# Kernel tuning notes

Measured on AMD Instinct MI355X. Metric: run time of the kernel, lower is better.

Reference implementation:

```python
import jax, jax.numpy as jnp
import numpy as np

N = 50000        # nodes
E = 1600000      # edges
NDIM_IN = 64
HID = 128        # hardcoded hidden width of first SAGELayer in E-GraphSAGE
NDIM_OUT = 128
EDIM = 32
EMBEDIM = 128
NCLASS = 2       # bin=True


def setup_inputs() -> dict:
    key = jax.random.key(0)
    ks = jax.random.split(key, 12)
    g = lambda k, shape: jax.random.normal(k, shape, jnp.float32) / np.sqrt(np.float32(shape[0]))
    return {
        "nfeats": jax.random.normal(ks[0], (N, NDIM_IN), jnp.float32),
        "efeats": jax.random.normal(ks[1], (E, EDIM), jnp.float32),
        "src": jax.random.randint(ks[2], (E,), 0, N),
        "dst": jax.random.randint(ks[3], (E,), 0, N),
        # SAGE layer 1: W_msg [ndim_in+edim -> 128], W_apply [ndim_in+128 -> 128]
        "Wm1": g(ks[4], (NDIM_IN + EDIM, HID)), "bm1": jnp.zeros((HID,), jnp.float32),
        "Wa1": g(ks[5], (NDIM_IN + HID, HID)), "ba1": jnp.zeros((HID,), jnp.float32),
        # SAGE layer 2: W_msg [128+edim -> ndim_out], W_apply [128+ndim_out -> ndim_out]
        "Wm2": g(ks[6], (HID + EDIM, NDIM_OUT)), "bm2": jnp.zeros((NDIM_OUT,), jnp.float32),
        "Wa2": g(ks[7], (HID + NDIM_OUT, NDIM_OUT)), "ba2": jnp.zeros((NDIM_OUT,), jnp.float32),
        # MLPPredictorEmbed: [2*ndim_out -> embedim] -> relu -> [embedim -> 2]
        "W1": g(ks[8], (2 * NDIM_OUT, EMBEDIM)), "b1": jnp.zeros((EMBEDIM,), jnp.float32),
        "W2": g(ks[9], (EMBEDIM, NCLASS)), "b2": jnp.zeros((NCLASS,), jnp.float32),
    }


def _sage_layer(h, efeats, src, dst, Wm, bm, Wa, ba):
    # per-edge message: relu(W_msg([h_src || e]))  -> [E, dout]
    m = jax.nn.relu(jnp.concatenate([h[src], efeats], axis=-1) @ Wm + bm)
    # mean aggregation by destination node (0 for isolated nodes, like DGL fn.mean)
    s = jax.ops.segment_sum(m, dst, num_segments=N)
    cnt = jax.ops.segment_sum(jnp.ones((m.shape[0], 1), m.dtype), dst, num_segments=N)
    h_neigh = s / jnp.maximum(cnt, 1.0)
    # node update: relu(W_apply([h || h_neigh]))
    return jax.nn.relu(jnp.concatenate([h, h_neigh], axis=-1) @ Wa + ba)


def reference(nfeats, efeats, src, dst,
              Wm1, bm1, Wa1, ba1, Wm2, bm2, Wa2, ba2,
              W1, b1, W2, b2):
    h = _sage_layer(nfeats, efeats, src, dst, Wm1, bm1, Wa1, ba1)   # [N, 128]
    h = _sage_layer(h, efeats, src, dst, Wm2, bm2, Wa2, ba2)        # [N, ndim_out]
    # edge predictor: MLP on [h_u || h_v] per edge
    z = jnp.concatenate([h[src], h[dst]], axis=-1)                   # [E, 2*ndim_out]
    score = jax.nn.relu(z @ W1 + b1) @ W2 + b2                       # [E, 2]
    return score
```

## Files before the change

kernel.cpp:

```cpp
#include <hip/hip_runtime.h>

#define N_NODES 50000
#define N_EDGES 1600000

typedef _Float16 h8 __attribute__((ext_vector_type(8)));
typedef float f4 __attribute__((ext_vector_type(4)));

__device__ inline h8 ld_h8(const _Float16* p) { return *(const h8*)p; }

__device__ inline h8 cvt2h8(f4 a, f4 b) {
    h8 r;
    r[0] = (_Float16)a[0]; r[1] = (_Float16)a[1]; r[2] = (_Float16)a[2]; r[3] = (_Float16)a[3];
    r[4] = (_Float16)b[0]; r[5] = (_Float16)b[1]; r[6] = (_Float16)b[2]; r[7] = (_Float16)b[3];
    return r;
}


__global__ void prep_weights(const float* __restrict__ Wm1, const float* __restrict__ Wa1,
                             const float* __restrict__ Wm2, const float* __restrict__ Wa2,
                             const float* __restrict__ W1,
                             _Float16* __restrict__ Wm1t, _Float16* __restrict__ Wa1t,
                             _Float16* __restrict__ Wm2t, _Float16* __restrict__ Wa2t,
                             _Float16* __restrict__ W1t)
{
    int i = blockIdx.x * 256 + threadIdx.x;
    if (i < 12288) {
        int o = i / 96, k = i % 96;
        int ks = k >> 5, q = (k >> 3) & 3, j = k & 7;
        int c = q ^ ((o >> 1) & 3);
        Wm1t[(ks * 128 + o) * 32 + c * 8 + j] = (_Float16)Wm1[k * 128 + o];
    } else if (i < 36864) {
        int jj = i - 12288; int o = jj / 192, k = jj % 192;
        Wa1t[o * 200 + k] = (_Float16)Wa1[k * 128 + o];
    } else if (i < 57344) {
        int jj = i - 36864; int o = jj / 160, k = jj % 160;
        int ks = k >> 5, q = (k >> 3) & 3, j = k & 7;
        int c = q ^ ((o >> 1) & 3);
        Wm2t[(ks * 128 + o) * 32 + c * 8 + j] = (_Float16)Wm2[k * 128 + o];
    } else if (i < 90112) {
        int jj = i - 57344; int o = jj >> 8, k = jj & 255;
        Wa2t[(o << 8) + k] = (_Float16)Wa2[k * 128 + o];
    } else if (i < 122880) {
        int jj = i - 90112; int o = jj >> 8, k = jj & 255;
        W1t[(o << 8) + k] = (_Float16)W1[k * 128 + o];
    }
}

__global__ void cvt_nfeats(const float* __restrict__ nf, _Float16* __restrict__ nf16)
{
    int i = blockIdx.x * 256 + threadIdx.x;
    nf16[i] = (_Float16)nf[i];
}


__global__ void hist_kernel(const int* __restrict__ dst, int* __restrict__ cnt)
{
    int e = blockIdx.x * 256 + threadIdx.x;
    atomicAdd(cnt + dst[e], 1);
}

__global__ void scan1_kernel(const int* __restrict__ cnt, int* __restrict__ tmp,
                             int* __restrict__ bsum)
{
    __shared__ int sh[256];
    int t = threadIdx.x, i = blockIdx.x * 256 + t;
    int v = (i < N_NODES) ? cnt[i] : 0;
    sh[t] = v; __syncthreads();
    for (int off = 1; off < 256; off <<= 1) {
        int x = (t >= off) ? sh[t - off] : 0;
        __syncthreads();
        sh[t] += x;
        __syncthreads();
    }
    if (i < N_NODES) tmp[i] = sh[t];
    if (t == 255) bsum[blockIdx.x] = sh[255];
}

__global__ void scan2_kernel(const int* __restrict__ bsum, int* __restrict__ bbase)
{
    __shared__ int sh[256];
    int t = threadIdx.x;
    int v = (t < 196) ? bsum[t] : 0;
    sh[t] = v; __syncthreads();
    for (int off = 1; off < 256; off <<= 1) {
        int x = (t >= off) ? sh[t - off] : 0;
        __syncthreads();
        sh[t] += x;
        __syncthreads();
    }
    if (t < 196) bbase[t] = sh[t] - v;
}

__global__ void scan3_kernel(const int* __restrict__ cnt, const int* __restrict__ tmp,
                             const int* __restrict__ bbase, int* __restrict__ cursor)
{
    int t = threadIdx.x, b = blockIdx.x, i = b * 256 + t;
    if (i < N_NODES) cursor[i] = tmp[i] - cnt[i] + bbase[b];
}

__global__ void scatter_kernel(const int* __restrict__ src, const int* __restrict__ dst,
                               int* __restrict__ cursor,
                               int2* __restrict__ pairs, int* __restrict__ dsts)
{
    int e = blockIdx.x * 256 + threadIdx.x;
    int d = dst[e];
    int pos = atomicAdd(cursor + d, 1);
    pairs[pos] = make_int2(e, src[e]);
    dsts[pos] = d;
}

template<int KSRC_H, int MINW>
__launch_bounds__(256, MINW)
__global__ void msg_kernel_sorted(const _Float16* __restrict__ ntab,
                                  const float* __restrict__ efeats,
                                  const int2* __restrict__ pairs,
                                  const int* __restrict__ dsts,
                                  const _Float16* __restrict__ Wt,
                                  const float* __restrict__ bias,
                                  float* __restrict__ sacc)
{
    constexpr int EFSTEP = KSRC_H / 32;
    constexpr int KSTEPS = EFSTEP + 1;
    constexpr int BH = (KSRC_H + 32) * 128;
    constexpr int BBYTES = BH * 2;
    constexpr int SCRBYTES = 4 * 16 * 132 * 4;
    constexpr int LDSBYTES = BBYTES > SCRBYTES ? BBYTES : SCRBYTES;
    __shared__ __align__(16) char smem[LDSBYTES];
    _Float16* Bsh = (_Float16*)smem;

    const int tid = threadIdx.x;
    const int wave = tid >> 6, lane = tid & 63;
    const int q = lane >> 4, l15 = lane & 15;
    const int wbase = blockIdx.x * 128 + wave * 32;

    const int2 p0 = pairs[wbase + l15];
    const int2 p1 = pairs[wbase + 16 + l15];
    const _Float16* r0 = ntab + (size_t)p0.y * KSRC_H + q * 8;
    const _Float16* r1 = ntab + (size_t)p1.y * KSRC_H + q * 8;
    h8 a0p = ld_h8(r0);
    h8 a1p = ld_h8(r1);
    const float* ep0 = efeats + (size_t)p0.x * 32 + q * 8;
    const float* ep1 = efeats + (size_t)p1.x * 32 + q * 8;
    f4 e0a, e0b, e1a, e1b;
    if constexpr (KSRC_H > 64) {
        e0a = *(const f4*)ep0; e0b = *(const f4*)(ep0 + 4);
        e1a = *(const f4*)ep1; e1b = *(const f4*)(ep1 + 4);
    }

    {
        const uint4* s4 = (const uint4*)Wt;
        uint4* d4 = (uint4*)smem;
        constexpr int n4 = BH / 8;
        for (int i = tid; i < n4; i += 256) d4[i] = s4[i];
    }
    __syncthreads();

    f4 acc[2][8];
#pragma unroll
    for (int t = 0; t < 2; t++)
#pragma unroll
        for (int nt = 0; nt < 8; nt++) acc[t][nt] = (f4){0.f, 0.f, 0.f, 0.f};

    const _Float16* bp = Bsh + l15 * 32 + ((q ^ ((l15 >> 1) & 3)) << 3);
#pragma unroll
    for (int ks = 0; ks < KSTEPS; ks++) {
        h8 a0, a1;
        if (ks == 0) {
            a0 = a0p; a1 = a1p;
        } else if (ks < EFSTEP) {
            a0 = ld_h8(r0 + ks * 32);
            a1 = ld_h8(r1 + ks * 32);
        } else {
            if constexpr (KSRC_H > 64) {
                a0 = cvt2h8(e0a, e0b);
                a1 = cvt2h8(e1a, e1b);
            } else {
                a0 = cvt2h8(*(const f4*)ep0, *(const f4*)(ep0 + 4));
                a1 = cvt2h8(*(const f4*)ep1, *(const f4*)(ep1 + 4));
            }
        }
#pragma unroll
        for (int nt = 0; nt < 8; nt++) {
            h8 b = ld_h8(bp + ks * 4096 + nt * 512);
            acc[0][nt] = __builtin_amdgcn_mfma_f32_16x16x32_f16(a0, b, acc[0][nt], 0, 0, 0);
            acc[1][nt] = __builtin_amdgcn_mfma_f32_16x16x32_f16(a1, b, acc[1][nt], 0, 0, 0);
        }
    }

    __syncthreads();

    float* wsch = (float*)smem + wave * 2112;

    float bv[8];
#pragma unroll
    for (int nt = 0; nt < 8; nt++) bv[nt] = bias[nt * 16 + l15];

    const int4 dv0 = *(const int4*)(dsts + wbase + q * 4);
    const int4 dv1 = *(const int4*)(dsts + wbase + 16 + q * 4);
    const int df0 = __shfl(dv0.x, l15, 64);
    const int dl0 = __shfl(dv0.w, 48 + l15, 64);
    const int df1 = __shfl(dv1.x, l15, 64);
    const int dl1 = __shfl(dv1.w, 48 + l15, 64);

    auto reduce16 = [&](const f4 (&a)[8], int df, int dl, int rbase) {
        if (df == dl) {
            float sv[8];
#pragma unroll
            for (int nt = 0; nt < 8; nt++) {
                float s = fmaxf(a[nt][0] + bv[nt], 0.f) + fmaxf(a[nt][1] + bv[nt], 0.f)
                        + fmaxf(a[nt][2] + bv[nt], 0.f) + fmaxf(a[nt][3] + bv[nt], 0.f);
                s += __shfl_xor(s, 16, 64);
                s += __shfl_xor(s, 32, 64);
                sv[nt] = s;
            }
#pragma unroll
            for (int i = 0; i < 2; i++) {
                float x = (q == 0) ? sv[i*4] : (q == 1) ? sv[i*4+1] : (q == 2) ? sv[i*4+2] : sv[i*4+3];
                atomicAdd(sacc + (size_t)df * 128 + i * 64 + lane, x);
            }
        } else {
#pragma unroll
            for (int nt = 0; nt < 8; nt++)
#pragma unroll
                for (int r = 0; r < 4; r++)
                    wsch[(q * 4 + r) * 132 + nt * 16 + l15] = fmaxf(a[nt][r] + bv[nt], 0.f);
            const int rb = __builtin_amdgcn_readfirstlane(rbase);
            float s0 = 0.f, s1 = 0.f;
            int dp = dsts[rb];
            for (int rr = 0; rr < 16; rr++) {
                const int d = dsts[rb + rr];
                const float v0 = wsch[rr * 132 + lane];
                const float v1 = wsch[rr * 132 + 64 + lane];
                if (d != dp) {
                    atomicAdd(sacc + (size_t)dp * 128 + lane, s0);
                    atomicAdd(sacc + (size_t)dp * 128 + 64 + lane, s1);
                    s0 = v0; s1 = v1; dp = d;
                } else {
                    s0 += v0; s1 += v1;
                }
            }
            atomicAdd(sacc + (size_t)dp * 128 + lane, s0);
            atomicAdd(sacc + (size_t)dp * 128 + 64 + lane, s1);
        }
    };

    if (df0 == dl1) {
        float sv[8];
#pragma unroll
        for (int nt = 0; nt < 8; nt++) {
            float s = fmaxf(acc[0][nt][0] + bv[nt], 0.f) + fmaxf(acc[0][nt][1] + bv[nt], 0.f)
                    + fmaxf(acc[0][nt][2] + bv[nt], 0.f) + fmaxf(acc[0][nt][3] + bv[nt], 0.f)
                    + fmaxf(acc[1][nt][0] + bv[nt], 0.f) + fmaxf(acc[1][nt][1] + bv[nt], 0.f)
                    + fmaxf(acc[1][nt][2] + bv[nt], 0.f) + fmaxf(acc[1][nt][3] + bv[nt], 0.f);
            s += __shfl_xor(s, 16, 64);
            s += __shfl_xor(s, 32, 64);
            sv[nt] = s;
        }
#pragma unroll
        for (int i = 0; i < 2; i++) {
            float x = (q == 0) ? sv[i*4] : (q == 1) ? sv[i*4+1] : (q == 2) ? sv[i*4+2] : sv[i*4+3];
            atomicAdd(sacc + (size_t)df0 * 128 + i * 64 + lane, x);
        }
    } else {
        reduce16(acc[0], df0, dl0, wbase);
        reduce16(acc[1], df1, dl1, wbase + 16);
    }
}

template<int KSRC_H, bool SWIZ, int KPAD>
__launch_bounds__(256)
__global__ void apply_kernel(const _Float16* __restrict__ ntab,
                             const float* __restrict__ sacc,
                             const int* __restrict__ cnt,
                             const _Float16* __restrict__ Wt,
                             const float* __restrict__ bias,
                             _Float16* __restrict__ outtab)
{
    constexpr int KSTEPS = (KSRC_H + 128) / 32;
    __shared__ __align__(16) _Float16 Bsh[128 * KPAD];

    const int tid = threadIdx.x;
    if (SWIZ) {
        const uint4* s4 = (const uint4*)Wt;
        uint4* d4 = (uint4*)Bsh;
        for (int i = tid; i < 4096; i += 256) {
            int n = i >> 5, c = i & 31;
            d4[(n << 5) | (c ^ (n & 31))] = s4[i];
        }
    } else {
        const uint4* s4 = (const uint4*)Wt;
        uint4* d4 = (uint4*)Bsh;
        constexpr int n4 = 128 * KPAD / 8;
        for (int i = tid; i < n4; i += 256) d4[i] = s4[i];
    }
    __syncthreads();

    const int wave = tid >> 6, lane = tid & 63;
    const int q = lane >> 4, l15 = lane & 15;
    const int nbase = blockIdx.x * 128 + wave * 32;

    const int n0 = nbase + l15, n1 = nbase + 16 + l15;
    const int n0c = min(n0, N_NODES - 1), n1c = min(n1, N_NODES - 1);
    const _Float16* r0 = ntab + (size_t)n0c * KSRC_H;
    const _Float16* r1 = ntab + (size_t)n1c * KSRC_H;
    const float rcp0 = 1.0f / fmaxf((float)cnt[n0c], 1.0f);
    const float rcp1 = 1.0f / fmaxf((float)cnt[n1c], 1.0f);

    f4 acc[2][8];
#pragma unroll
    for (int t = 0; t < 2; t++)
#pragma unroll
        for (int nt = 0; nt < 8; nt++) acc[t][nt] = (f4){0.f, 0.f, 0.f, 0.f};

#pragma unroll
    for (int ks = 0; ks < KSTEPS; ks++) {
        h8 a0, a1;
        if (ks < KSRC_H / 32) {
            a0 = ld_h8(r0 + ks * 32 + q * 8);
            a1 = ld_h8(r1 + ks * 32 + q * 8);
        } else {
            const int kk = ks * 32 - KSRC_H + q * 8;
            const float* p0 = sacc + (size_t)n0c * 128 + kk;
            const float* p1 = sacc + (size_t)n1c * 128 + kk;
            f4 u0 = *(const f4*)p0 * rcp0, v0 = *(const f4*)(p0 + 4) * rcp0;
            f4 u1 = *(const f4*)p1 * rcp1, v1 = *(const f4*)(p1 + 4) * rcp1;
            a0 = cvt2h8(u0, v0);
            a1 = cvt2h8(u1, v1);
        }
#pragma unroll
        for (int nt = 0; nt < 8; nt++) {
            h8 b;
            if (SWIZ) {
                const int nrow = nt * 16 + l15;
                const int chunk = ((ks << 2) | q) ^ (nrow & 31);
                b = ld_h8(Bsh + (((nrow << 5) | chunk) << 3));
            } else {
                b = ld_h8(&Bsh[(nt * 16 + l15) * KPAD + ks * 32 + q * 8]);
            }
            acc[0][nt] = __builtin_amdgcn_mfma_f32_16x16x32_f16(a0, b, acc[0][nt], 0, 0, 0);
            acc[1][nt] = __builtin_amdgcn_mfma_f32_16x16x32_f16(a1, b, acc[1][nt], 0, 0, 0);
        }
    }

#pragma unroll
    for (int nt = 0; nt < 8; nt++) {
        const int col = nt * 16 + l15;
        const float bv = bias[col];
#pragma unroll
        for (int t = 0; t < 2; t++)
#pragma unroll
            for (int r = 0; r < 4; r++) {
                const int node = nbase + t * 16 + q * 4 + r;
                if (node < N_NODES) {
                    float v = fmaxf(acc[t][nt][r] + bv, 0.f);
                    outtab[(size_t)node * 128 + col] = (_Float16)v;
                }
            }
    }
}

__launch_bounds__(256)
__global__ void pred_kernel(const _Float16* __restrict__ h2,
                            const int* __restrict__ src,
                            const int* __restrict__ dst,
                            const _Float16* __restrict__ W1t,
                            const float* __restrict__ b1,
                            const float* __restrict__ W2,
                            const float* __restrict__ b2,
                            float* __restrict__ out)
{
    __shared__ __align__(16) _Float16 Bsh[128 * 256];

    const int tid = threadIdx.x;
    {
        const uint4* s4 = (const uint4*)W1t;
        uint4* d4 = (uint4*)Bsh;
        for (int i = tid; i < 4096; i += 256) {
            int n = i >> 5, c = i & 31;
            d4[(n << 5) | (c ^ (n & 31))] = s4[i];
        }
    }
    __syncthreads();

    const int wave = tid >> 6, lane = tid & 63;
    const int q = lane >> 4, l15 = lane & 15;
    const int ebase = blockIdx.x * 128 + wave * 32;

    const int e0 = ebase + l15, e1 = ebase + 16 + l15;
    const _Float16* rs0 = h2 + (size_t)src[e0] * 128;
    const _Float16* rd0 = h2 + (size_t)dst[e0] * 128;
    const _Float16* rs1 = h2 + (size_t)src[e1] * 128;
    const _Float16* rd1 = h2 + (size_t)dst[e1] * 128;

    f4 acc[2][8];
#pragma unroll
    for (int t = 0; t < 2; t++)
#pragma unroll
        for (int nt = 0; nt < 8; nt++) acc[t][nt] = (f4){0.f, 0.f, 0.f, 0.f};

#pragma unroll
    for (int ks = 0; ks < 8; ks++) {
        h8 a0, a1;
        if (ks < 4) {
            a0 = ld_h8(rs0 + ks * 32 + q * 8);
            a1 = ld_h8(rs1 + ks * 32 + q * 8);
        } else {
            a0 = ld_h8(rd0 + (ks - 4) * 32 + q * 8);
            a1 = ld_h8(rd1 + (ks - 4) * 32 + q * 8);
        }
#pragma unroll
        for (int nt = 0; nt < 8; nt++) {
            const int nrow = nt * 16 + l15;
            const int chunk = ((ks << 2) | q) ^ (nrow & 31);
            h8 b = ld_h8(Bsh + (((nrow << 5) | chunk) << 3));
            acc[0][nt] = __builtin_amdgcn_mfma_f32_16x16x32_f16(a0, b, acc[0][nt], 0, 0, 0);
            acc[1][nt] = __builtin_amdgcn_mfma_f32_16x16x32_f16(a1, b, acc[1][nt], 0, 0, 0);
        }
    }

    float o[2][4][2];
#pragma unroll
    for (int t = 0; t < 2; t++)
#pragma unroll
        for (int r = 0; r < 4; r++) { o[t][r][0] = 0.f; o[t][r][1] = 0.f; }

#pragma unroll
    for (int nt = 0; nt < 8; nt++) {
        const int nrow = nt * 16 + l15;
        const float bv = b1[nrow];
        const float w20 = W2[nrow * 2 + 0];
        const float w21 = W2[nrow * 2 + 1];
#pragma unroll
        for (int t = 0; t < 2; t++)
#pragma unroll
            for (int r = 0; r < 4; r++) {
                float y = fmaxf(acc[t][nt][r] + bv, 0.f);
                o[t][r][0] += y * w20;
                o[t][r][1] += y * w21;
            }
    }

#pragma unroll
    for (int m = 1; m < 16; m <<= 1) {
#pragma unroll
        for (int t = 0; t < 2; t++)
#pragma unroll
            for (int r = 0; r < 4; r++) {
                o[t][r][0] += __shfl_xor(o[t][r][0], m, 64);
                o[t][r][1] += __shfl_xor(o[t][r][1], m, 64);
            }
    }

    if (l15 < 8) {
        const int r = l15 >> 1, c = l15 & 1;
        const float bb = c ? b2[1] : b2[0];
#pragma unroll
        for (int t = 0; t < 2; t++) {
            float v0 = (r == 0) ? o[t][0][0] : (r == 1) ? o[t][1][0] : (r == 2) ? o[t][2][0] : o[t][3][0];
            float v1 = (r == 0) ? o[t][0][1] : (r == 1) ? o[t][1][1] : (r == 2) ? o[t][2][1] : o[t][3][1];
            float v = (c ? v1 : v0) + bb;
            out[(size_t)(ebase + t * 16 + q * 4 + r) * 2 + c] = v;
        }
    }
}


extern "C" void kernel_launch(void* const* d_in, const int* in_sizes, int n_in,
                              void* d_out, int out_size, void* d_ws, size_t ws_size,
                              hipStream_t stream)
{
    const float* nfeats = (const float*)d_in[0];
    const float* efeats = (const float*)d_in[1];
    const int*   src    = (const int*)d_in[2];
    const int*   dst    = (const int*)d_in[3];
    const float* Wm1 = (const float*)d_in[4],  *bm1 = (const float*)d_in[5];
    const float* Wa1 = (const float*)d_in[6],  *ba1 = (const float*)d_in[7];
    const float* Wm2 = (const float*)d_in[8],  *bm2 = (const float*)d_in[9];
    const float* Wa2 = (const float*)d_in[10], *ba2 = (const float*)d_in[11];
    const float* W1  = (const float*)d_in[12], *b1  = (const float*)d_in[13];
    const float* W2  = (const float*)d_in[14], *b2  = (const float*)d_in[15];
    float* out = (float*)d_out;

    char* ws = (char*)d_ws;
    float*     s     = (float*)(ws);
    int*       cnt   = (int*)(ws + 25600000);
    int*       tmp   = (int*)(ws + 25800000);
    int*       cursor= (int*)(ws + 26000000);
    int*       bsum  = (int*)(ws + 26200000);
    int*       bbase = (int*)(ws + 26201024);
    _Float16*  nf16  = (_Float16*)(ws + 26202048);
    int2*      pairs = (int2*)(ws + 32602048);
    int*       dsts  = (int*)(ws + 45402048);
    _Float16*  h1    = (_Float16*)(ws + 51802048);
    _Float16*  h2    = (_Float16*)(ws + 26202048);
    _Float16*  Wm1t  = (_Float16*)(ws + 64602048);
    _Float16*  Wa1t  = (_Float16*)(ws + 64626624);
    _Float16*  Wm2t  = (_Float16*)(ws + 64677824);
    _Float16*  Wa2t  = (_Float16*)(ws + 64718784);
    _Float16*  W1t   = (_Float16*)(ws + 64784320);

    hipMemsetAsync(s, 0, 25600000, stream);
    hipMemsetAsync(cnt, 0, 200000, stream);

    prep_weights<<<480, 256, 0, stream>>>(Wm1, Wa1, Wm2, Wa2, W1, Wm1t, Wa1t, Wm2t, Wa2t, W1t);
    cvt_nfeats<<<12500, 256, 0, stream>>>(nfeats, nf16);

    hist_kernel<<<6250, 256, 0, stream>>>(dst, cnt);
    scan1_kernel<<<196, 256, 0, stream>>>(cnt, tmp, bsum);
    scan2_kernel<<<1, 256, 0, stream>>>(bsum, bbase);
    scan3_kernel<<<196, 256, 0, stream>>>(cnt, tmp, bbase, cursor);
    scatter_kernel<<<6250, 256, 0, stream>>>(src, dst, cursor, pairs, dsts);

    msg_kernel_sorted<64, 5><<<12500, 256, 0, stream>>>(nf16, efeats, pairs, dsts, Wm1t, bm1, s);
    apply_kernel<64, false, 200><<<391, 256, 0, stream>>>(nf16, s, cnt, Wa1t, ba1, h1);

    hipMemsetAsync(s, 0, 25600000, stream);
    msg_kernel_sorted<128, 4><<<12500, 256, 0, stream>>>(h1, efeats, pairs, dsts, Wm2t, bm2, s);
    apply_kernel<128, true, 256><<<391, 256, 0, stream>>>(h1, s, cnt, Wa2t, ba2, h2);

    pred_kernel<<<12500, 256, 0, stream>>>(h2, src, dst, W1t, b1, W2, b2, out);
}
```

Before: 1.105 ms.

## Run edge predictor over destination-sorted edges with half-size shared weight tiles

Adds a predictor kernel that walks edges in the destination-sorted order already built for aggregation, so the h2 gathers for destinations hit cache better. Each half of W1 is staged into shared memory in turn, halving LDS use so more blocks can be resident, and results are scattered back through the original edge ids. It needs a larger workspace to keep h2 from overlapping the pairs/dsts buffers and falls back to the old kernel otherwise. Output writes become scattered instead of contiguous, and the kernel now has extra barriers.

```diff
diff --git a/kernel.cpp b/kernel.cpp
--- a/kernel.cpp
+++ b/kernel.cpp
@@ -359,6 +359,140 @@
     }
 }
 
+__launch_bounds__(256, 4)
+__global__ void pred_kernel_sorted(const _Float16* __restrict__ h2,
+                                   const int2* __restrict__ pairs,
+                                   const int* __restrict__ dsts,
+                                   const _Float16* __restrict__ W1t,
+                                   const float* __restrict__ b1,
+                                   const float* __restrict__ W2,
+                                   const float* __restrict__ b2,
+                                   float* __restrict__ out)
+{
+    __shared__ __align__(16) _Float16 Bsh[128 * 128];
+
+    const int tid = threadIdx.x;
+    const int wave = tid >> 6, lane = tid & 63;
+    const int q = lane >> 4, l15 = lane & 15;
+    const int ebase = blockIdx.x * 128 + wave * 32;
+
+    const int2 p0 = pairs[ebase + l15];
+    const int2 p1 = pairs[ebase + 16 + l15];
+    const _Float16* rs0 = h2 + (size_t)p0.y * 128 + q * 8;
+    const _Float16* rs1 = h2 + (size_t)p1.y * 128 + q * 8;
+    h8 s0p = ld_h8(rs0);
+    h8 s1p = ld_h8(rs1);
+    const int d0 = dsts[ebase + l15];
+    const int d1 = dsts[ebase + 16 + l15];
+    const _Float16* rd0 = h2 + (size_t)d0 * 128 + q * 8;
+    const _Float16* rd1 = h2 + (size_t)d1 * 128 + q * 8;
+
+    {
+        const uint4* s4 = (const uint4*)W1t;
+        uint4* d4 = (uint4*)Bsh;
+        for (int i = tid; i < 2048; i += 256) {
+            int n = i >> 4, c = i & 15;
+            d4[(n << 4) | (c ^ (n & 15))] = s4[n * 32 + c];
+        }
+    }
+    __syncthreads();
+
+    f4 acc[2][8];
+#pragma unroll
+    for (int t = 0; t < 2; t++)
+#pragma unroll
+        for (int nt = 0; nt < 8; nt++) acc[t][nt] = (f4){0.f, 0.f, 0.f, 0.f};
+
+#pragma unroll
+    for (int ks = 0; ks < 4; ks++) {
+        h8 a0 = (ks == 0) ? s0p : ld_h8(rs0 + ks * 32);
+        h8 a1 = (ks == 0) ? s1p : ld_h8(rs1 + ks * 32);
+#pragma unroll
+        for (int nt = 0; nt < 8; nt++) {
+            const int nrow = nt * 16 + l15;
+            const int chunk = ((ks << 2) | q) ^ (nrow & 15);
+            h8 b = ld_h8(Bsh + (((nrow << 4) | chunk) << 3));
+            acc[0][nt] = __builtin_amdgcn_mfma_f32_16x16x32_f16(a0, b, acc[0][nt], 0, 0, 0);
+            acc[1][nt] = __builtin_amdgcn_mfma_f32_16x16x32_f16(a1, b, acc[1][nt], 0, 0, 0);
+        }
+    }
+
+    h8 d0p = ld_h8(rd0);
+    h8 d1p = ld_h8(rd1);
+
+    __syncthreads();
+
+    {
+        const uint4* s4 = (const uint4*)W1t;
+        uint4* d4 = (uint4*)Bsh;
+        for (int i = tid; i < 2048; i += 256) {
+            int n = i >> 4, c = i & 15;
+            d4[(n << 4) | (c ^ (n & 15))] = s4[n * 32 + 16 + c];
+        }
+    }
+    __syncthreads();
+
+#pragma unroll
+    for (int ks = 0; ks < 4; ks++) {
+        h8 a0 = (ks == 0) ? d0p : ld_h8(rd0 + ks * 32);
+        h8 a1 = (ks == 0) ? d1p : ld_h8(rd1 + ks * 32);
+#pragma unroll
+        for (int nt = 0; nt < 8; nt++) {
+            const int nrow = nt * 16 + l15;
+            const int chunk = ((ks << 2) | q) ^ (nrow & 15);
+            h8 b = ld_h8(Bsh + (((nrow << 4) | chunk) << 3));
+            acc[0][nt] = __builtin_amdgcn_mfma_f32_16x16x32_f16(a0, b, acc[0][nt], 0, 0, 0);
+            acc[1][nt] = __builtin_amdgcn_mfma_f32_16x16x32_f16(a1, b, acc[1][nt], 0, 0, 0);
+        }
+    }
+
+    float o[2][4][2];
+#pragma unroll
+    for (int t = 0; t < 2; t++)
+#pragma unroll
+        for (int r = 0; r < 4; r++) { o[t][r][0] = 0.f; o[t][r][1] = 0.f; }
+
+#pragma unroll
+    for (int nt = 0; nt < 8; nt++) {
+        const int nrow = nt * 16 + l15;
+        const float bv = b1[nrow];
+        const float w20 = W2[nrow * 2 + 0];
+        const float w21 = W2[nrow * 2 + 1];
+#pragma unroll
+        for (int t = 0; t < 2; t++)
+#pragma unroll
+            for (int r = 0; r < 4; r++) {
+                float y = fmaxf(acc[t][nt][r] + bv, 0.f);
+                o[t][r][0] += y * w20;
+                o[t][r][1] += y * w21;
+            }
+    }
+
+#pragma unroll
+    for (int m = 1; m < 16; m <<= 1) {
+#pragma unroll
+        for (int t = 0; t < 2; t++)
+#pragma unroll
+            for (int r = 0; r < 4; r++) {
+                o[t][r][0] += __shfl_xor(o[t][r][0], m, 64);
+                o[t][r][1] += __shfl_xor(o[t][r][1], m, 64);
+            }
+    }
+
+    if (l15 < 8) {
+        const int r = l15 >> 1, c = l15 & 1;
+        const float bb = c ? b2[1] : b2[0];
+#pragma unroll
+        for (int t = 0; t < 2; t++) {
+            float v0 = (r == 0) ? o[t][0][0] : (r == 1) ? o[t][1][0] : (r == 2) ? o[t][2][0] : o[t][3][0];
+            float v1 = (r == 0) ? o[t][0][1] : (r == 1) ? o[t][1][1] : (r == 2) ? o[t][2][1] : o[t][3][1];
+            float v = (c ? v1 : v0) + bb;
+            const int e = pairs[ebase + t * 16 + q * 4 + r].x;
+            out[(size_t)e * 2 + c] = v;
+        }
+    }
+}
+
 __launch_bounds__(256)
 __global__ void pred_kernel(const _Float16* __restrict__ h2,
                             const int* __restrict__ src,
@@ -492,13 +626,16 @@
     int2*      pairs = (int2*)(ws + 32602048);
     int*       dsts  = (int*)(ws + 45402048);
     _Float16*  h1    = (_Float16*)(ws + 51802048);
-    _Float16*  h2    = (_Float16*)(ws + 26202048);
     _Float16*  Wm1t  = (_Float16*)(ws + 64602048);
     _Float16*  Wa1t  = (_Float16*)(ws + 64626624);
     _Float16*  Wm2t  = (_Float16*)(ws + 64677824);
     _Float16*  Wa2t  = (_Float16*)(ws + 64718784);
     _Float16*  W1t   = (_Float16*)(ws + 64784320);
 
+    const bool big_ws = ws_size >= (size_t)77800000;
+    _Float16* h2 = big_ws ? (_Float16*)(ws + 64849920)
+                          : (_Float16*)(ws + 26202048);
+
     hipMemsetAsync(s, 0, 25600000, stream);
     hipMemsetAsync(cnt, 0, 200000, stream);
 
@@ -518,5 +655,8 @@
     msg_kernel_sorted<128, 4><<<12500, 256, 0, stream>>>(h1, efeats, pairs, dsts, Wm2t, bm2, s);
     apply_kernel<128, true, 256><<<391, 256, 0, stream>>>(h1, s, cnt, Wa2t, ba2, h2);
 
-    pred_kernel<<<12500, 256, 0, stream>>>(h2, src, dst, W1t, b1, W2, b2, out);
-}
+    if (big_ws)
+        pred_kernel_sorted<<<12500, 256, 0, stream>>>(h2, pairs, dsts, W1t, b1, W2, b2, out);
+    else
+        pred_kernel<<<12500, 256, 0, stream>>>(h2, src, dst, W1t, b1, W2, b2, out);
+}
```

Result: faster. 1.043 ms (-5.6%).

## Factor edge-predictor first layer into per-node projections before per-edge combine

Applied to the files above, without the earlier changes.

The first predictor layer is linear in [h_src || h_dst], so it is split into per-node products P = h·W1_top and Q = h·W1_bottom + b1, computed once per node with MFMA. A per-edge elementwise kernel then gathers P[src] and Q[dst], applies relu and the 128x2 output layer. This removes the per-edge 256x128 GEMM and walks edges in dst-sorted order so the Q gathers stay local. The cost is extra gather traffic for fp16 P and fp32 Q, a larger workspace requirement, and a fallback to the old path when the workspace is too small.

```diff
diff --git a/kernel.cpp b/kernel.cpp
--- a/kernel.cpp
+++ b/kernel.cpp
@@ -360,6 +360,131 @@
 }
 
 __launch_bounds__(256)
+__global__ void node_pq_kernel(const _Float16* __restrict__ h2,
+                               const _Float16* __restrict__ W1t,
+                               const float* __restrict__ b1,
+                               _Float16* __restrict__ P,
+                               float* __restrict__ Q)
+{
+    __shared__ __align__(16) _Float16 Bsh[128 * 256];
+
+    const int tid = threadIdx.x;
+    {
+        const uint4* s4 = (const uint4*)W1t;
+        uint4* d4 = (uint4*)Bsh;
+        for (int i = tid; i < 4096; i += 256) {
+            int n = i >> 5, c = i & 31;
+            d4[(n << 5) | (c ^ (n & 31))] = s4[i];
+        }
+    }
+    __syncthreads();
+
+    const int wave = tid >> 6, lane = tid & 63;
+    const int q = lane >> 4, l15 = lane & 15;
+    const int nbase = blockIdx.x * 128 + wave * 32;
+
+    const int n0 = nbase + l15, n1 = nbase + 16 + l15;
+    const int n0c = min(n0, N_NODES - 1), n1c = min(n1, N_NODES - 1);
+    const _Float16* r0 = h2 + (size_t)n0c * 128;
+    const _Float16* r1 = h2 + (size_t)n1c * 128;
+
+    f4 accP[2][8], accQ[2][8];
+#pragma unroll
+    for (int t = 0; t < 2; t++)
+#pragma unroll
+        for (int nt = 0; nt < 8; nt++) {
+            accP[t][nt] = (f4){0.f, 0.f, 0.f, 0.f};
+            accQ[t][nt] = (f4){0.f, 0.f, 0.f, 0.f};
+        }
+
+#pragma unroll
+    for (int ks = 0; ks < 4; ks++) {
+        h8 a0 = ld_h8(r0 + ks * 32 + q * 8);
+        h8 a1 = ld_h8(r1 + ks * 32 + q * 8);
+#pragma unroll
+        for (int nt = 0; nt < 8; nt++) {
+            const int nrow = nt * 16 + l15;
+            const int cP = ((ks << 2) | q) ^ (nrow & 31);
+            h8 bP = ld_h8(Bsh + (((nrow << 5) | cP) << 3));
+            accP[0][nt] = __builtin_amdgcn_mfma_f32_16x16x32_f16(a0, bP, accP[0][nt], 0, 0, 0);
+            accP[1][nt] = __builtin_amdgcn_mfma_f32_16x16x32_f16(a1, bP, accP[1][nt], 0, 0, 0);
+            const int cQ = (((ks + 4) << 2) | q) ^ (nrow & 31);
+            h8 bQ = ld_h8(Bsh + (((nrow << 5) | cQ) << 3));
+            accQ[0][nt] = __builtin_amdgcn_mfma_f32_16x16x32_f16(a0, bQ, accQ[0][nt], 0, 0, 0);
+            accQ[1][nt] = __builtin_amdgcn_mfma_f32_16x16x32_f16(a1, bQ, accQ[1][nt], 0, 0, 0);
+        }
+    }
+
+#pragma unroll
+    for (int nt = 0; nt < 8; nt++) {
+        const int col = nt * 16 + l15;
+        const float bq = b1[col];
+#pragma unroll
+        for (int t = 0; t < 2; t++)
+#pragma unroll
+            for (int r = 0; r < 4; r++) {
+                const int node = nbase + t * 16 + q * 4 + r;
+                if (node < N_NODES) {
+                    P[(size_t)node * 128 + col] = (_Float16)accP[t][nt][r];
+                    Q[(size_t)node * 128 + col] = accQ[t][nt][r] + bq;
+                }
+            }
+    }
+}
+
+__launch_bounds__(256, 4)
+__global__ void pred_elem_kernel(const _Float16* __restrict__ P,
+                                 const float* __restrict__ Q,
+                                 const int2* __restrict__ pairs,
+                                 const int* __restrict__ dsts,
+                                 const float* __restrict__ W2,
+                                 const float* __restrict__ b2,
+                                 float* __restrict__ out)
+{
+    __shared__ __align__(16) float w20sh[128];
+    __shared__ __align__(16) float w21sh[128];
+
+    const int tid = threadIdx.x;
+    if (tid < 128) {
+        w20sh[tid] = W2[tid * 2 + 0];
+        w21sh[tid] = W2[tid * 2 + 1];
+    }
+    __syncthreads();
+
+    const int slot = blockIdx.x * 256 + tid;
+    const int2 pr = pairs[slot];
+    const int d = dsts[slot];
+    const _Float16* prow = P + (size_t)pr.y * 128;
+    const float* qrow = Q + (size_t)d * 128;
+
+    float o0 = 0.f, o1 = 0.f;
+#pragma unroll
+    for (int c = 0; c < 4; c++) {
+        h8 pv[4];
+#pragma unroll
+        for (int i = 0; i < 4; i++) pv[i] = ld_h8(prow + c * 32 + i * 8);
+        f4 qv[8];
+#pragma unroll
+        for (int i = 0; i < 8; i++) qv[i] = *(const f4*)(qrow + c * 32 + i * 4);
+#pragma unroll
+        for (int i = 0; i < 8; i++) {
+            const f4 w0 = *(const f4*)(w20sh + c * 32 + i * 4);
+            const f4 w1 = *(const f4*)(w21sh + c * 32 + i * 4);
+#pragma unroll
+            for (int j = 0; j < 4; j++) {
+                const float pvf = (float)pv[i >> 1][(i & 1) * 4 + j];
+                const float y = fmaxf(pvf + qv[i][j], 0.f);
+                o0 += y * w0[j];
+                o1 += y * w1[j];
+            }
+        }
+    }
+
+    out[(size_t)pr.x * 2 + 0] = o0 + b2[0];
+    out[(size_t)pr.x * 2 + 1] = o1 + b2[1];
+}
+
+__launch_bounds__(256)
 __global__ void pred_kernel(const _Float16* __restrict__ h2,
                             const int* __restrict__ src,
                             const int* __restrict__ dst,
@@ -492,13 +617,16 @@
     int2*      pairs = (int2*)(ws + 32602048);
     int*       dsts  = (int*)(ws + 45402048);
     _Float16*  h1    = (_Float16*)(ws + 51802048);
-    _Float16*  h2    = (_Float16*)(ws + 26202048);
     _Float16*  Wm1t  = (_Float16*)(ws + 64602048);
     _Float16*  Wa1t  = (_Float16*)(ws + 64626624);
     _Float16*  Wm2t  = (_Float16*)(ws + 64677824);
     _Float16*  Wa2t  = (_Float16*)(ws + 64718784);
     _Float16*  W1t   = (_Float16*)(ws + 64784320);
 
+    const bool big_ws = ws_size >= (size_t)77800000;
+    _Float16* h2 = big_ws ? (_Float16*)(ws + 64849920)
+                          : (_Float16*)(ws + 26202048);
+
     hipMemsetAsync(s, 0, 25600000, stream);
     hipMemsetAsync(cnt, 0, 200000, stream);
 
@@ -518,5 +646,12 @@
     msg_kernel_sorted<128, 4><<<12500, 256, 0, stream>>>(h1, efeats, pairs, dsts, Wm2t, bm2, s);
     apply_kernel<128, true, 256><<<391, 256, 0, stream>>>(h1, s, cnt, Wa2t, ba2, h2);
 
-    pred_kernel<<<12500, 256, 0, stream>>>(h2, src, dst, W1t, b1, W2, b2, out);
-}
+    if (big_ws) {
+        _Float16* P = h1;
+        float*    Q = s;
+        node_pq_kernel<<<391, 256, 0, stream>>>(h2, W1t, b1, P, Q);
+        pred_elem_kernel<<<6250, 256, 0, stream>>>(P, Q, pairs, dsts, W2, b2, out);
+    } else {
+        pred_kernel<<<12500, 256, 0, stream>>>(h2, src, dst, W1t, b1, W2, b2, out);
+    }
+}
```

Measured after the change: 1.021 ms. 1.08x faster.
